# Optimization experiments

Measured on AMD Instinct MI355X. Metric: run time of the kernel, lower is better.

## Reference

```python
import jax, jax.numpy as jnp
import numpy as np

B, N, IN_DIM, H, D = 4, 2048, 128, 4, 64
NEG_SLOPE = 0.2
MASK_VAL = -1e9


def setup_inputs() -> dict:
    key = jax.random.key(0)
    k1, k2, k3, k4, k5 = jax.random.split(key, 5)
    x = jax.random.normal(k1, (B, N, IN_DIM), dtype=jnp.float32)
    adj = jax.random.randint(k2, (N, N), 0, 2, dtype=jnp.int32)
    W = jax.random.normal(k3, (H * D, IN_DIM), dtype=jnp.float32) * 0.05
    att_src = jax.random.normal(k4, (1, H, D), dtype=jnp.float32) * 0.05
    att_dst = jax.random.normal(k5, (1, H, D), dtype=jnp.float32) * 0.05
    return {"x": x, "adj": adj, "W": W, "att_src": att_src, "att_dst": att_dst}


def reference(x, adj, W, att_src, att_dst):
    # linear (no bias), torch layout: y = x @ W.T  -> [B,N,H*D]
    h = jnp.einsum('bni,oi->bno', x, W).reshape(B, N, H, D).transpose(0, 2, 1, 3)  # [B,H,N,D]
    e_src = jnp.einsum('bhnd,hd->bhn', h, att_src[0])  # [B,H,N]
    e_dst = jnp.einsum('bhnd,hd->bhn', h, att_dst[0])  # [B,H,N]
    # additive score: e[b,h,i,j] = leaky_relu(e_src[b,h,i] + e_dst[b,h,j])
    e = jax.nn.leaky_relu(e_src[..., :, None] + e_dst[..., None, :], NEG_SLOPE)  # [B,H,N,N]
    e = jnp.where(adj[None, None] <= 0, MASK_VAL, e)
    attn = jax.nn.softmax(e, axis=-1)  # dropout inactive (inference)
    out = jnp.einsum('bhij,bhjd->bhid', attn, h)  # [B,H,N,D]
    return out.transpose(0, 2, 1, 3).reshape(B, N, H * D)  # concat heads
```

## Files before the change

kernel.cpp:

```cpp
#include <hip/hip_runtime.h>


#define NDIM 2048
#define NEG_SLOPE 0.2f
#define LOG2E 1.4426950408889634f

typedef __bf16 bf16x8 __attribute__((ext_vector_type(8)));
typedef __bf16 bf16x4 __attribute__((ext_vector_type(4)));
typedef float  f32x4  __attribute__((ext_vector_type(4)));

#define LP 136

__device__ static inline void load_lds16(const void* g, void* l) {
    __builtin_amdgcn_global_load_lds(
        (const __attribute__((address_space(1))) unsigned*)g,
        (__attribute__((address_space(3))) unsigned*)l, 16, 0, 0);
}

__global__ __launch_bounds__(256) void adj_pack(const int* __restrict__ adj,
                                                unsigned* __restrict__ bits) {
    const int t = threadIdx.x;
    const int q = blockIdx.x * 256 + t;
    int4 a = ((const int4*)adj)[q];
    unsigned nib = (unsigned)(a.x > 0) | ((unsigned)(a.y > 0) << 1) |
                   ((unsigned)(a.z > 0) << 2) | ((unsigned)(a.w > 0) << 3);
    unsigned v = nib << ((t & 7) * 4);
    v |= __shfl_xor(v, 1, 64);
    v |= __shfl_xor(v, 2, 64);
    v |= __shfl_xor(v, 4, 64);
    if ((t & 7) == 0) bits[q >> 3] = v;
}

__global__ __launch_bounds__(256) void gat_linear(
    const float* __restrict__ x, const float* __restrict__ W,
    const float* __restrict__ att_src, const float* __restrict__ att_dst,
    __bf16* __restrict__ h_t, float* __restrict__ es_ws, float* __restrict__ ed_ws)
{
    const int t    = threadIdx.x;
    const int head = blockIdx.x & 3;
    const int n0g  = (blockIdx.x >> 2) * 64;
    const int b    = n0g >> 11;
    const int n0   = n0g & (NDIM - 1);
    const int bh   = b * 4 + head;

    __shared__ __align__(16) __bf16 Wl[64][LP];
    __shared__ __align__(16) __bf16 Xl[64][LP];

    #pragma unroll
    for (int i = 0; i < 8; ++i) {
        int idx = t + i * 256;
        int r = idx >> 5, c4 = idx & 31;
        float4 wv = *((const float4*)(W + (size_t)(head * 64 + r) * 128) + c4);
        bf16x4 bv;
        bv[0] = (__bf16)wv.x; bv[1] = (__bf16)wv.y; bv[2] = (__bf16)wv.z; bv[3] = (__bf16)wv.w;
        *(bf16x4*)&Wl[r][c4 * 4] = bv;
    }
    #pragma unroll
    for (int i = 0; i < 8; ++i) {
        int idx = t + i * 256;
        int r = idx >> 5, c4 = idx & 31;
        float4 xv = *((const float4*)(x + (size_t)(n0g + r) * 128) + c4);
        bf16x4 bv;
        bv[0] = (__bf16)xv.x; bv[1] = (__bf16)xv.y; bv[2] = (__bf16)xv.z; bv[3] = (__bf16)xv.w;
        *(bf16x4*)&Xl[r][c4 * 4] = bv;
    }
    __syncthreads();

    const int lane = t & 63, w = t >> 6;
    const int m = lane & 15, q4 = lane >> 4;

    bf16x8 bfr[4];
    #pragma unroll
    for (int ks = 0; ks < 4; ++ks)
        bfr[ks] = *(const bf16x8*)&Xl[w * 16 + m][ks * 32 + q4 * 8];

    f32x4 acc[4];
    #pragma unroll
    for (int c = 0; c < 4; ++c) acc[c] = (f32x4){0.f, 0.f, 0.f, 0.f};

    #pragma unroll
    for (int ct = 0; ct < 4; ++ct) {
        #pragma unroll
        for (int ks = 0; ks < 4; ++ks) {
            bf16x8 afr = *(const bf16x8*)&Wl[ct * 16 + m][ks * 32 + q4 * 8];
            acc[ct] = __builtin_amdgcn_mfma_f32_16x16x32_bf16(afr, bfr[ks], acc[ct], 0, 0, 0);
        }
    }

    const int nloc = n0 + w * 16 + m;
    float esA = 0.f, edA = 0.f;
    #pragma unroll
    for (int ct = 0; ct < 4; ++ct) {
        float4 aS = *(const float4*)(att_src + head * 64 + ct * 16 + q4 * 4);
        float4 aD = *(const float4*)(att_dst + head * 64 + ct * 16 + q4 * 4);
        #pragma unroll
        for (int r = 0; r < 4; ++r) {
            float v = acc[ct][r];
            int   d = ct * 16 + q4 * 4 + r;
            h_t[(size_t)(bh * 64 + d) * NDIM + nloc] = (__bf16)v;
            esA += v * ((const float*)&aS)[r];
            edA += v * ((const float*)&aD)[r];
        }
    }
    esA += __shfl_xor(esA, 16, 64); esA += __shfl_xor(esA, 32, 64);
    edA += __shfl_xor(edA, 16, 64); edA += __shfl_xor(edA, 32, 64);
    if (lane < 16) {
        es_ws[bh * NDIM + nloc] = esA * LOG2E;
        ed_ws[bh * NDIM + nloc] = edA * LOG2E;
    }
}

__global__ __launch_bounds__(256) void gat_attn(
    const unsigned long long* __restrict__ bits, const __bf16* __restrict__ h_t,
    const float* __restrict__ es_ws, const float* __restrict__ ed_ws,
    float* __restrict__ out)
{
    const int blk = blockIdx.x;
    const int bh  = blk & 15;
    const int i0  = (blk >> 4) * 64;
    const int t   = threadIdx.x;
    const int lane = t & 63, w = t >> 6;
    const int m = lane & 15, q4 = lane >> 4;

    __shared__ __align__(16) __bf16 Hl[2][64][64];

    const int r0 = w * 16 + (lane >> 3);
    const int r1 = r0 + 8;
    const int c8 = lane & 7;
    const __bf16* g0 = h_t + ((size_t)(bh * 64 + r0)) * NDIM + ((c8 ^ (r0 & 7)) * 8);
    const __bf16* g1 = h_t + ((size_t)(bh * 64 + r1)) * NDIM + ((c8 ^ (r1 & 7)) * 8);
    __bf16* l0a = &Hl[0][r0][c8 * 8];
    __bf16* l0b = &Hl[0][r1][c8 * 8];
    __bf16* l1a = &Hl[1][r0][c8 * 8];
    __bf16* l1b = &Hl[1][r1][c8 * 8];

    const float es2 = es_ws[bh * NDIM + i0 + w * 16 + m];
    const unsigned long long* brow = bits + (size_t)(i0 + w * 16 + m) * 32;
    const float* edp = ed_ws + bh * NDIM + q4 * 8;

    load_lds16(g0, l0a);
    load_lds16(g1, l0b);
    float eb[2][16];
    unsigned long long bwb[2];
    #pragma unroll
    for (int g = 0; g < 4; ++g)
        *(float4*)&eb[0][g * 4] = *(const float4*)(edp + (g >> 1) * 32 + (g & 1) * 4);
    bwb[0] = brow[0];

    f32x4 acc[4], accl;
    #pragma unroll
    for (int c = 0; c < 4; ++c) acc[c] = (f32x4){0.f, 0.f, 0.f, 0.f};
    accl = (f32x4){0.f, 0.f, 0.f, 0.f};
    bf16x8 ones;
    #pragma unroll
    for (int jj = 0; jj < 8; ++jj) ones[jj] = (__bf16)1.0f;
    const int sw = m & 7;

    __syncthreads();

#define STEP(ITJ, P)                                                            \
    {                                                                           \
        const int itj = (ITJ);                                                  \
        if (itj < 31) {                                                         \
            load_lds16(g0 + (itj + 1) * 64, (P) ? l0a : l1a);                   \
            load_lds16(g1 + (itj + 1) * 64, (P) ? l0b : l1b);                   \
            const float* ep = edp + (itj + 1) * 64;                             \
            _Pragma("unroll")                                                   \
            for (int g = 0; g < 4; ++g)                                         \
                *(float4*)&eb[(P) ^ 1][g * 4] =                                 \
                    *(const float4*)(ep + (g >> 1) * 32 + (g & 1) * 4);         \
            bwb[(P) ^ 1] = brow[itj + 1];                                       \
        }                                                                       \
        bf16x8 af[2];                                                           \
        _Pragma("unroll")                                                       \
        for (int ks = 0; ks < 2; ++ks) {                                        \
            unsigned bm = (unsigned)(bwb[P] >> (ks * 32 + q4 * 8)) & 0xFFu;     \
            _Pragma("unroll")                                                   \
            for (int jj = 0; jj < 8; ++jj) {                                    \
                float s = es2 + eb[P][ks * 8 + jj];                             \
                s = fmaxf(s, NEG_SLOPE * s);                                    \
                s = ((bm >> jj) & 1u) ? s : -10000.0f;                          \
                af[ks][jj] = (__bf16)__builtin_amdgcn_exp2f(s);                 \
            }                                                                   \
        }                                                                       \
        _Pragma("unroll")                                                       \
        for (int ks = 0; ks < 2; ++ks) {                                        \
            accl = __builtin_amdgcn_mfma_f32_16x16x32_bf16(af[ks], ones, accl, 0, 0, 0); \
            _Pragma("unroll")                                                   \
            for (int ct = 0; ct < 4; ++ct) {                                    \
                bf16x8 bfr = *(const bf16x8*)&Hl[P][ct * 16 + m][(((ks * 4 + q4) ^ sw)) * 8]; \
                acc[ct] = __builtin_amdgcn_mfma_f32_16x16x32_bf16(af[ks], bfr, acc[ct], 0, 0, 0); \
            }                                                                   \
        }                                                                       \
        __syncthreads();                                                        \
    }

    for (int it2 = 0; it2 < 16; ++it2) {
        STEP(it2 * 2, 0);
        STEP(it2 * 2 + 1, 1);
    }
#undef STEP

    float invr[4];
    #pragma unroll
    for (int r = 0; r < 4; ++r) invr[r] = 1.f / accl[r];

    const int b = bh >> 2, head = bh & 3;
    float* ob = out + ((size_t)(b * NDIM + i0 + w * 16)) * 256 + head * 64;
    #pragma unroll
    for (int ct = 0; ct < 4; ++ct) {
        #pragma unroll
        for (int r = 0; r < 4; ++r) {
            ob[(size_t)(q4 * 4 + r) * 256 + ct * 16 + m] = acc[ct][r] * invr[r];
        }
    }
}

extern "C" void kernel_launch(void* const* d_in, const int* in_sizes, int n_in,
                              void* d_out, int out_size, void* d_ws, size_t ws_size,
                              hipStream_t stream) {
    const float* x       = (const float*)d_in[0];
    const int*   adj     = (const int*)d_in[1];
    const float* W       = (const float*)d_in[2];
    const float* att_src = (const float*)d_in[3];
    const float* att_dst = (const float*)d_in[4];
    float* out = (float*)d_out;

    __bf16*   h_t   = (__bf16*)d_ws;
    float*    es_ws = (float*)((char*)d_ws + (size_t)4 * 1024 * 1024);
    float*    ed_ws = es_ws + 16 * NDIM;
    unsigned* bitsp = (unsigned*)(ed_ws + 16 * NDIM);

    adj_pack<<<NDIM * NDIM / 4 / 256, 256, 0, stream>>>(adj, bitsp);
    gat_linear<<<512, 256, 0, stream>>>(x, W, att_src, att_dst, h_t, es_ws, ed_ws);
    gat_attn<<<512, 256, 0, stream>>>((const unsigned long long*)bitsp, h_t, es_ws, ed_ws, out);
}
```

Before: 108.2 us.

## Fuse adjacency bit-packing into linear kernel and use 32x32 MFMA tiles in attention

Removes the separate adj_pack launch by packing the adjacency bits inside gat_linear, with each of the 512 blocks handling 2048 int4 groups. The attention kernel moves from 16x16x32 to 32x32x16 bf16 MFMA, so each wave covers 32 rows and each block 128 rows. This halves the grid and the number of times each H tile is reloaded per row. The aim is fewer launches and more reuse of the shared H tiles per MFMA, at the cost of more registers per wave and half as many blocks to fill the GPU.

```diff
diff --git a/kernel.cpp b/kernel.cpp
--- a/kernel.cpp
+++ b/kernel.cpp
@@ -8,6 +8,7 @@
 typedef __bf16 bf16x8 __attribute__((ext_vector_type(8)));
 typedef __bf16 bf16x4 __attribute__((ext_vector_type(4)));
 typedef float  f32x4  __attribute__((ext_vector_type(4)));
+typedef float  f32x16 __attribute__((ext_vector_type(16)));
 
 #define LP 136
 
@@ -17,23 +18,10 @@
         (__attribute__((address_space(3))) unsigned*)l, 16, 0, 0);
 }
 
-__global__ __launch_bounds__(256) void adj_pack(const int* __restrict__ adj,
-                                                unsigned* __restrict__ bits) {
-    const int t = threadIdx.x;
-    const int q = blockIdx.x * 256 + t;
-    int4 a = ((const int4*)adj)[q];
-    unsigned nib = (unsigned)(a.x > 0) | ((unsigned)(a.y > 0) << 1) |
-                   ((unsigned)(a.z > 0) << 2) | ((unsigned)(a.w > 0) << 3);
-    unsigned v = nib << ((t & 7) * 4);
-    v |= __shfl_xor(v, 1, 64);
-    v |= __shfl_xor(v, 2, 64);
-    v |= __shfl_xor(v, 4, 64);
-    if ((t & 7) == 0) bits[q >> 3] = v;
-}
-
 __global__ __launch_bounds__(256) void gat_linear(
     const float* __restrict__ x, const float* __restrict__ W,
     const float* __restrict__ att_src, const float* __restrict__ att_dst,
+    const int* __restrict__ adj, unsigned* __restrict__ bits,
     __bf16* __restrict__ h_t, float* __restrict__ es_ws, float* __restrict__ ed_ws)
 {
     const int t    = threadIdx.x;
@@ -46,6 +34,11 @@
     __shared__ __align__(16) __bf16 Wl[64][LP];
     __shared__ __align__(16) __bf16 Xl[64][LP];
 
+    int4 ap[8];
+    #pragma unroll
+    for (int i = 0; i < 8; ++i)
+        ap[i] = ((const int4*)adj)[blockIdx.x * 2048 + i * 256 + t];
+
     #pragma unroll
     for (int i = 0; i < 8; ++i) {
         int idx = t + i * 256;
@@ -63,6 +56,18 @@
         bf16x4 bv;
         bv[0] = (__bf16)xv.x; bv[1] = (__bf16)xv.y; bv[2] = (__bf16)xv.z; bv[3] = (__bf16)xv.w;
         *(bf16x4*)&Xl[r][c4 * 4] = bv;
+    }
+
+    #pragma unroll
+    for (int i = 0; i < 8; ++i) {
+        int q = blockIdx.x * 2048 + i * 256 + t;
+        unsigned nib = (unsigned)(ap[i].x > 0) | ((unsigned)(ap[i].y > 0) << 1) |
+                       ((unsigned)(ap[i].z > 0) << 2) | ((unsigned)(ap[i].w > 0) << 3);
+        unsigned v = nib << ((t & 7) * 4);
+        v |= __shfl_xor(v, 1, 64);
+        v |= __shfl_xor(v, 2, 64);
+        v |= __shfl_xor(v, 4, 64);
+        if ((t & 7) == 0) bits[q >> 3] = v;
     }
     __syncthreads();
 
@@ -117,10 +122,11 @@
 {
     const int blk = blockIdx.x;
     const int bh  = blk & 15;
-    const int i0  = (blk >> 4) * 64;
+    const int i0  = (blk >> 4) * 128;
     const int t   = threadIdx.x;
     const int lane = t & 63, w = t >> 6;
-    const int m = lane & 15, q4 = lane >> 4;
+    const int m32 = lane & 31, q = lane >> 5;
+    const int sw  = m32 & 7;
 
     __shared__ __align__(16) __bf16 Hl[2][64][64];
 
@@ -134,27 +140,28 @@
     __bf16* l1a = &Hl[1][r0][c8 * 8];
     __bf16* l1b = &Hl[1][r1][c8 * 8];
 
-    const float es2 = es_ws[bh * NDIM + i0 + w * 16 + m];
-    const unsigned long long* brow = bits + (size_t)(i0 + w * 16 + m) * 32;
-    const float* edp = ed_ws + bh * NDIM + q4 * 8;
+    const int irow = i0 + w * 32 + m32;
+    const float es2 = es_ws[bh * NDIM + irow];
+    const unsigned long long* brow = bits + (size_t)irow * 32;
+    const float* edp = ed_ws + bh * NDIM + q * 8;
 
     load_lds16(g0, l0a);
     load_lds16(g1, l0b);
-    float eb[2][16];
+    float eb[2][32] __attribute__((aligned(16)));
     unsigned long long bwb[2];
     #pragma unroll
-    for (int g = 0; g < 4; ++g)
-        *(float4*)&eb[0][g * 4] = *(const float4*)(edp + (g >> 1) * 32 + (g & 1) * 4);
+    for (int ks = 0; ks < 4; ++ks) {
+        *(float4*)&eb[0][ks * 8]     = *(const float4*)(edp + ks * 16);
+        *(float4*)&eb[0][ks * 8 + 4] = *(const float4*)(edp + ks * 16 + 4);
+    }
     bwb[0] = brow[0];
 
-    f32x4 acc[4], accl;
-    #pragma unroll
-    for (int c = 0; c < 4; ++c) acc[c] = (f32x4){0.f, 0.f, 0.f, 0.f};
-    accl = (f32x4){0.f, 0.f, 0.f, 0.f};
+    f32x16 acc0 = {0.f}, acc1 = {0.f}, accl = {0.f};
+    #pragma unroll
+    for (int e = 0; e < 16; ++e) { acc0[e] = 0.f; acc1[e] = 0.f; accl[e] = 0.f; }
     bf16x8 ones;
     #pragma unroll
     for (int jj = 0; jj < 8; ++jj) ones[jj] = (__bf16)1.0f;
-    const int sw = m & 7;
 
     __syncthreads();
 
@@ -166,15 +173,16 @@
             load_lds16(g1 + (itj + 1) * 64, (P) ? l0b : l1b);                   \
             const float* ep = edp + (itj + 1) * 64;                             \
             _Pragma("unroll")                                                   \
-            for (int g = 0; g < 4; ++g)                                         \
-                *(float4*)&eb[(P) ^ 1][g * 4] =                                 \
-                    *(const float4*)(ep + (g >> 1) * 32 + (g & 1) * 4);         \
+            for (int ks = 0; ks < 4; ++ks) {                                    \
+                *(float4*)&eb[(P) ^ 1][ks * 8]     = *(const float4*)(ep + ks * 16);     \
+                *(float4*)&eb[(P) ^ 1][ks * 8 + 4] = *(const float4*)(ep + ks * 16 + 4); \
+            }                                                                   \
             bwb[(P) ^ 1] = brow[itj + 1];                                       \
         }                                                                       \
-        bf16x8 af[2];                                                           \
+        bf16x8 af[4];                                                           \
         _Pragma("unroll")                                                       \
-        for (int ks = 0; ks < 2; ++ks) {                                        \
-            unsigned bm = (unsigned)(bwb[P] >> (ks * 32 + q4 * 8)) & 0xFFu;     \
+        for (int ks = 0; ks < 4; ++ks) {                                        \
+            unsigned bm = (unsigned)(bwb[P] >> (ks * 16 + q * 8)) & 0xFFu;      \
             _Pragma("unroll")                                                   \
             for (int jj = 0; jj < 8; ++jj) {                                    \
                 float s = es2 + eb[P][ks * 8 + jj];                             \
@@ -184,13 +192,12 @@
             }                                                                   \
         }                                                                       \
         _Pragma("unroll")                                                       \
-        for (int ks = 0; ks < 2; ++ks) {                                        \
-            accl = __builtin_amdgcn_mfma_f32_16x16x32_bf16(af[ks], ones, accl, 0, 0, 0); \
-            _Pragma("unroll")                                                   \
-            for (int ct = 0; ct < 4; ++ct) {                                    \
-                bf16x8 bfr = *(const bf16x8*)&Hl[P][ct * 16 + m][(((ks * 4 + q4) ^ sw)) * 8]; \
-                acc[ct] = __builtin_amdgcn_mfma_f32_16x16x32_bf16(af[ks], bfr, acc[ct], 0, 0, 0); \
-            }                                                                   \
+        for (int ks = 0; ks < 4; ++ks) {                                        \
+            accl = __builtin_amdgcn_mfma_f32_32x32x16_bf16(af[ks], ones, accl, 0, 0, 0); \
+            bf16x8 b0 = *(const bf16x8*)&Hl[P][m32][(((ks * 2 + q) ^ sw)) * 8];          \
+            acc0 = __builtin_amdgcn_mfma_f32_32x32x16_bf16(af[ks], b0, acc0, 0, 0, 0);   \
+            bf16x8 b1 = *(const bf16x8*)&Hl[P][32 + m32][(((ks * 2 + q) ^ sw)) * 8];     \
+            acc1 = __builtin_amdgcn_mfma_f32_32x32x16_bf16(af[ks], b1, acc1, 0, 0, 0);   \
         }                                                                       \
         __syncthreads();                                                        \
     }
@@ -201,18 +208,14 @@
     }
 #undef STEP
 
-    float invr[4];
-    #pragma unroll
-    for (int r = 0; r < 4; ++r) invr[r] = 1.f / accl[r];
-
     const int b = bh >> 2, head = bh & 3;
-    float* ob = out + ((size_t)(b * NDIM + i0 + w * 16)) * 256 + head * 64;
-    #pragma unroll
-    for (int ct = 0; ct < 4; ++ct) {
-        #pragma unroll
-        for (int r = 0; r < 4; ++r) {
-            ob[(size_t)(q4 * 4 + r) * 256 + ct * 16 + m] = acc[ct][r] * invr[r];
-        }
+    #pragma unroll
+    for (int reg = 0; reg < 16; ++reg) {
+        const int r = (reg & 3) + 8 * (reg >> 2) + 4 * q;
+        const float inv = 1.f / accl[reg];
+        float* op = out + ((size_t)(b * NDIM + i0 + w * 32 + r)) * 256 + head * 64 + m32;
+        op[0]  = acc0[reg] * inv;
+        op[32] = acc1[reg] * inv;
     }
 }
 
@@ -231,7 +234,8 @@
     float*    ed_ws = es_ws + 16 * NDIM;
     unsigned* bitsp = (unsigned*)(ed_ws + 16 * NDIM);
 
-    adj_pack<<<NDIM * NDIM / 4 / 256, 256, 0, stream>>>(adj, bitsp);
-    gat_linear<<<512, 256, 0, stream>>>(x, W, att_src, att_dst, h_t, es_ws, ed_ws);
-    gat_attn<<<512, 256, 0, stream>>>((const unsigned long long*)bitsp, h_t, es_ws, ed_ws, out);
-}
+    gat_linear<<<512, 256, 0, stream>>>(x, W, att_src, att_dst, adj, bitsp,
+                                        h_t, es_ws, ed_ws);
+    gat_attn<<<256, 256, 0, stream>>>((const unsigned long long*)bitsp,
+                                      h_t, es_ws, ed_ws, out);
+}
```

Result: slower. 112.9 us (+4.3%).
